# Optimization experiments

Hardware: AMD Instinct MI355X
Metric: run time of the kernel (lower is better)

## Reference

```python
import jax, jax.numpy as jnp
import numpy as np
import math

PATCH = 16
IMG = 224
HEADS = 12
EMB = 768
HEAD_DIM = EMB // HEADS
SCALE = 1.0 / math.sqrt(HEAD_DIM)
NEG = -1.0e9


def _make_masks():
    n = IMG // PATCH  # patches per side
    centers = np.arange(n) * PATCH + PATCH / 2.0
    rows = np.repeat(centers, n)  # token center rows, length n*n
    cols = np.tile(centers, n)    # token center cols
    left = (cols[:, None] < cols[None, :]).astype(np.float32)
    right = (cols[:, None] > cols[None, :]).astype(np.float32)
    up = (rows[:, None] < rows[None, :]).astype(np.float32)
    down = (rows[:, None] > rows[None, :]).astype(np.float32)
    ident = np.eye(n * n, dtype=np.float32)
    pad = lambda m: np.pad(m, ((1, 0), (1, 0)))  # prepend CLS row/col of zeros
    return [jnp.asarray(pad(m)) for m in (left, right, up, down, ident)]

MASKS = _make_masks()  # 5 masks, each [N, N] with N = 197


def setup_inputs() -> dict:
    key = jax.random.key(0)
    ks = jax.random.split(key, 18)
    B, N = 32, (IMG // PATCH) ** 2 + 1
    w = lambda k: jax.random.normal(k, (EMB, EMB), jnp.float32) * 0.02
    b = lambda k: jax.random.normal(k, (EMB,), jnp.float32) * 0.02
    return {
        'x': jax.random.normal(ks[0], (B, N, EMB), jnp.float32),
        'q_w': w(ks[1]), 'q_b': b(ks[2]),
        'kA_w': w(ks[3]), 'kA_b': b(ks[4]),
        'kB_w': w(ks[5]), 'kB_b': b(ks[6]),
        'kC_w': w(ks[7]), 'kC_b': b(ks[8]),
        'kD_w': w(ks[9]), 'kD_b': b(ks[10]),
        'kE_w': w(ks[11]), 'kE_b': b(ks[12]),
        'v_w': w(ks[13]), 'v_b': b(ks[14]),
        'proj_w': w(ks[15]), 'proj_b': b(ks[16]),
    }


def reference(x, q_w, q_b, kA_w, kA_b, kB_w, kB_b, kC_w, kC_b, kD_w, kD_b,
              kE_w, kE_b, v_w, v_b, proj_w, proj_b):
    B, N, _ = x.shape
    # torch Linear: y = x @ W.T + b; then [B,N,H,D] -> [B,H,N,D]
    lin = lambda w, b_: (x @ w.T + b_).reshape(B, N, HEADS, HEAD_DIM).transpose(0, 2, 1, 3)
    q = lin(q_w, q_b) * SCALE
    v = lin(v_w, v_b)
    out = jnp.zeros_like(v)
    k_params = [(kA_w, kA_b), (kB_w, kB_b), (kC_w, kC_b), (kD_w, kD_b), (kE_w, kE_b)]
    for (kw, kb), mask in zip(k_params, MASKS):
        k = lin(kw, kb)
        scores = jnp.einsum('bhnd,bhmd->bhnm', q, k) + (1.0 - mask) * NEG
        out = out + jnp.einsum('bhnm,bhmd->bhnd', jax.nn.softmax(scores, axis=-1), v)
    out = out.transpose(0, 2, 1, 3).reshape(B, N, EMB)
    return out @ proj_w.T + proj_b
```

## Files before the change

### kernel.cpp

```cpp
#include <hip/hip_runtime.h>
#include <stdint.h>

typedef unsigned short u16;
typedef __bf16 bf16x8 __attribute__((ext_vector_type(8)));
typedef float f32x4 __attribute__((ext_vector_type(4)));

#define KDIM   768
#define MP     6400
#define MREAL  6304
#define SLOT   ((size_t)MP * KDIM)
#define WSZ    ((size_t)KDIM * KDIM)
#define QSCALE_L 0.18033688011112042f
#define BIGL     1.4426950e9f

struct Ptr9 { const float* p[9]; };
struct Ptr7 { const float* p[7]; };

__device__ __forceinline__ u16 f2b(float f) {
  uint32_t x = __float_as_uint(f);
  x += 0x7FFFu + ((x >> 16) & 1u);
  return (u16)(x >> 16);
}

__device__ __forceinline__ float b2f(u16 v) {
  return __uint_as_float(((uint32_t)v) << 16);
}

__device__ __forceinline__ void async16(const void* g, void* l) {
  __builtin_amdgcn_global_load_lds(
      (__attribute__((address_space(1))) void*)(uintptr_t)g,
      (__attribute__((address_space(3))) void*)l, 16, 0, 0);
}

__global__ __launch_bounds__(256) void k_convert(Ptr9 src, u16* __restrict__ xb,
                                                 u16* __restrict__ wall) {
  const int XN4 = MREAL * KDIM / 4;
  const int WN4 = (int)(WSZ / 4);
  const int total = XN4 + 8 * WN4;
  for (int i = blockIdx.x * blockDim.x + threadIdx.x; i < total;
       i += gridDim.x * blockDim.x) {
    const float4* sp; ushort4* dp; int off;
    if (i < XN4) { sp = (const float4*)src.p[0]; dp = (ushort4*)xb; off = i; }
    else {
      int t = i - XN4; int slot = t / WN4; off = t - slot * WN4;
      sp = (const float4*)src.p[1 + slot];
      dp = (ushort4*)(wall + (size_t)slot * WSZ);
    }
    float4 v = sp[off];
    ushort4 u;
    u.x = f2b(v.x); u.y = f2b(v.y); u.z = f2b(v.z); u.w = f2b(v.w);
    dp[off] = u;
  }
}

__global__ __launch_bounds__(256) void k_gemm(const u16* __restrict__ A,
                                              const u16* __restrict__ W,
                                              Ptr7 bias,
                                              u16* __restrict__ outb,
                                              float* __restrict__ outf,
                                              float scale0, int guard) {
  __shared__ u16 As[128 * 32];
  __shared__ u16 Bs[128 * 32];
  const int tid = threadIdx.x;
  const int w = tid >> 6, lane = tid & 63;
  const int li = lane & 15, g = lane >> 4;
  const int brow = blockIdx.x, bcol = blockIdx.y, z = blockIdx.z;
  const u16* Wz = W + (size_t)z * WSZ;
  const float* bz = bias.p[z];
  const int wr = (w >> 1) * 64, wc = (w & 1) * 64;
  f32x4 acc[4][4] = {};

  for (int k0 = 0; k0 < KDIM; k0 += 32) {
    __syncthreads();
#pragma unroll
    for (int c = 0; c < 2; ++c) {
      int cbase = (c * 4 + w) * 64;
      int chunk = cbase + lane;
      int row = chunk >> 2, kg = chunk & 3;
      async16(A  + (size_t)(brow * 128 + row) * KDIM + k0 + kg * 8,
              (char*)As + cbase * 16);
      async16(Wz + (size_t)(bcol * 128 + row) * KDIM + k0 + kg * 8,
              (char*)Bs + cbase * 16);
    }
    asm volatile("s_waitcnt vmcnt(0)" ::: "memory");
    __syncthreads();

    bf16x8 af[4], bfr[4];
#pragma unroll
    for (int i = 0; i < 4; ++i) {
      af[i]  = *(const bf16x8*)(As + (wr + i * 16 + li) * 32 + g * 8);
      bfr[i] = *(const bf16x8*)(Bs + (wc + i * 16 + li) * 32 + g * 8);
    }
#pragma unroll
    for (int i = 0; i < 4; ++i)
#pragma unroll
      for (int j = 0; j < 4; ++j)
        acc[i][j] = __builtin_amdgcn_mfma_f32_16x16x32_bf16(af[i], bfr[j],
                                                            acc[i][j], 0, 0, 0);
  }

  const float scz = (z == 0) ? scale0 : 1.0f;
  if (outf == nullptr) {
    u16* O = outb + (size_t)z * SLOT;
#pragma unroll
    for (int j = 0; j < 4; ++j) {
      int col = bcol * 128 + wc + j * 16 + li;
      float bsv = bz[col];
#pragma unroll
      for (int i = 0; i < 4; ++i) {
        int row = brow * 128 + wr + i * 16 + g * 4;
#pragma unroll
        for (int r = 0; r < 4; ++r)
          O[(size_t)(row + r) * KDIM + col] = f2b((acc[i][j][r] + bsv) * scz);
      }
    }
  } else {
#pragma unroll
    for (int j = 0; j < 4; ++j) {
      int col = bcol * 128 + wc + j * 16 + li;
      float bsv = bz[col];
#pragma unroll
      for (int i = 0; i < 4; ++i) {
        int row = brow * 128 + wr + i * 16 + g * 4;
#pragma unroll
        for (int r = 0; r < 4; ++r)
          if (row + r < guard)
            outf[(size_t)(row + r) * KDIM + col] = acc[i][j][r] + bsv;
      }
    }
  }
}

__global__ __launch_bounds__(512, 4) void k_attn(const u16* __restrict__ qkv,
                                                 u16* __restrict__ att) {
  __shared__ u16 KL[208 * 64];
  __shared__ u16 VT[64][228];
  __shared__ u16 P[2][8][16][36];
  const int tid = threadIdx.x;
  const int w = tid >> 6, lane = tid & 63;
  const int li = lane & 15, g = lane >> 4;
  const int bx = blockIdx.x, h = blockIdx.y, b = blockIdx.z;
  const int rt = bx * 8 + w;
  const size_t rowbase = (size_t)b * 197;
  const int cb = h * 64;
  const u16* Q = qkv;
  const u16* V = qkv + 6 * SLOT;
  const bool task = (rt <= 12);
  const int nmask = (bx == 0) ? 5 : 4;

  auto stageK = [&](int m) {
    const u16* Kg = qkv + (size_t)(1 + m) * SLOT;
#pragma unroll
    for (int i = 0; i < 4; ++i) {
      int cb64 = (i * 8 + w) * 64;
      if (cb64 >= 1664) break;
      int c = cb64 + lane;
      int row = c >> 3;
      int kg = (c & 7) ^ (row & 7);
      async16(Kg + (rowbase + row) * KDIM + cb + kg * 8,
              (char*)KL + cb64 * 16);
    }
  };

  stageK(0);

  for (int e = tid; e < 64 * 228; e += 512) {
    int j = e >> 6, d = e & 63;
    u16 val = 0;
    if (j < 197) val = V[(rowbase + j) * KDIM + cb + d];
    VT[d][j] = val;
  }

  const int i_ = rt * 16 + li;
  const int pi = i_ - 1;
  const int ri = pi / 14, ci = pi % 14;
  const bool i0 = (i_ == 0);

  const int rs_init = (g * 4 - 1) / 14;
  const int cs_init = (g * 4 - 1) % 14;

  uint32_t b0l = 0, b0h = 0, b1l = 0, b1h = 0, b2l = 0, b2h = 0,
           b3l = 0, b3h = 0, b4l = 0, b4h = 0;
  {
    int cs = cs_init, rs = rs_init;
#pragma unroll
    for (int t = 0; t < 13; ++t) {
      int jv = t * 16 + g * 4;
      int cjr = cs, rjr = rs;
#pragma unroll
      for (int r = 0; r < 4; ++r) {
        const bool ok = (jv != 0) && !i0;
        const bool k0 = (ci < cjr) && ok;
        const bool k1 = (ci > cjr) && ok;
        const bool k2 = (ri < rjr) && ok;
        const bool k3 = (ri > rjr) && ok;
        const bool k4 = (i_ == jv) && ok;
        const int e = t * 4 + r;
        const uint32_t bit = 1u << (e & 31);
        if (e < 32) {
          b0l |= k0 ? bit : 0u; b1l |= k1 ? bit : 0u; b2l |= k2 ? bit : 0u;
          b3l |= k3 ? bit : 0u; b4l |= k4 ? bit : 0u;
        } else {
          b0h |= k0 ? bit : 0u; b1h |= k1 ? bit : 0u; b2h |= k2 ? bit : 0u;
          b3h |= k3 ? bit : 0u; b4h |= k4 ? bit : 0u;
        }
        ++jv; ++cjr; if (cjr == 14) { cjr = 0; ++rjr; }
      }
      cs += 2; ++rs; if (cs >= 14) { cs -= 14; ++rs; }
    }
  }

  bf16x8 qa0, qa1;
  {
    const size_t qrow = rowbase + (size_t)rt * 16 + li;
    qa0 = *(const bf16x8*)(Q + qrow * KDIM + cb + g * 8);
    qa1 = *(const bf16x8*)(Q + qrow * KDIM + cb + 32 + g * 8);
  }

  f32x4 oacc[4] = {};

  for (int m = 0; m < nmask; ++m) {
    asm volatile("s_waitcnt vmcnt(0)" ::: "memory");
    __syncthreads();

    const bool doit = task && (m < 4 || rt == 0);
    f32x4 s[13];
    if (doit) {
      __builtin_amdgcn_s_setprio(1);
#pragma unroll
      for (int t = 0; t < 13; ++t) {
        const char* base = (const char*)KL + (size_t)(t * 16 + li) * 128;
        const int sw = (li & 7) << 4;
        bf16x8 kb0 = *(const bf16x8*)(base + ((g * 16) ^ sw));
        bf16x8 kb1 = *(const bf16x8*)(base + ((64 + g * 16) ^ sw));
        f32x4 zz = {};
        zz = __builtin_amdgcn_mfma_f32_16x16x32_bf16(kb0, qa0, zz, 0, 0, 0);
        zz = __builtin_amdgcn_mfma_f32_16x16x32_bf16(kb1, qa1, zz, 0, 0, 0);
        s[t] = zz;
      }
      __builtin_amdgcn_s_setprio(0);
    }
    __syncthreads();
    if (m + 1 < nmask) stageK(m + 1);

    if (doit) {
      uint32_t wlo, whi;
      if (m == 0)      { wlo = b0l; whi = b0h; }
      else if (m == 1) { wlo = b1l; whi = b1h; }
      else if (m == 2) { wlo = b2l; whi = b2h; }
      else if (m == 3) { wlo = b3l; whi = b3h; }
      else             { wlo = b4l; whi = b4h; }

      float mx = -3.0e38f;
#pragma unroll
      for (int t = 0; t < 13; ++t) {
#pragma unroll
        for (int r = 0; r < 4; ++r) {
          const int e = t * 4 + r;
          const uint32_t w32 = (e < 32) ? wlo : whi;
          const bool mk = ((w32 >> (e & 31)) & 1u) != 0u;
          const int jv = t * 16 + g * 4 + r;
          float sv = s[t][r] - (mk ? 0.f : BIGL);
          if (jv >= 197) sv = -3.0e38f;
          s[t][r] = sv;
          mx = fmaxf(mx, sv);
        }
      }
      mx = fmaxf(mx, __shfl_xor(mx, 16));
      mx = fmaxf(mx, __shfl_xor(mx, 32));
      float sum = 0.f;
#pragma unroll
      for (int t = 0; t < 13; ++t)
#pragma unroll
        for (int r = 0; r < 4; ++r) {
          float e_ = exp2f(s[t][r] - mx);
          s[t][r] = e_;
          sum += e_;
        }
      sum += __shfl_xor(sum, 16);
      sum += __shfl_xor(sum, 32);
      const float inv = 1.0f / sum;

#pragma unroll
      for (int kt = 0; kt <= 7; ++kt) {
        if (kt < 7) {
#pragma unroll
          for (int h2 = 0; h2 < 2; ++h2) {
            const int t = kt * 2 + h2;
            uint32_t w0 = 0, w1 = 0;
            if (t < 13) {
              float a0 = s[t][0] * inv, a1 = s[t][1] * inv;
              float a2 = s[t][2] * inv, a3 = s[t][3] * inv;
              asm("v_cvt_pk_bf16_f32 %0, %1, %2" : "=v"(w0) : "v"(a0), "v"(a1));
              asm("v_cvt_pk_bf16_f32 %0, %1, %2" : "=v"(w1) : "v"(a2), "v"(a3));
            }
            uint2 pw; pw.x = w0; pw.y = w1;
            *(uint2*)&P[kt & 1][w][li][h2 * 16 + g * 4] = pw;
          }
        }
        if (kt > 0) {
          const int kr = kt - 1;
          bf16x8 pa = *(const bf16x8*)&P[kr & 1][w][li][g * 8];
          __builtin_amdgcn_s_setprio(1);
#pragma unroll
          for (int dt = 0; dt < 4; ++dt) {
            bf16x8 vb = *(const bf16x8*)&VT[dt * 16 + li][kr * 32 + g * 8];
            oacc[dt] = __builtin_amdgcn_mfma_f32_16x16x32_bf16(pa, vb, oacc[dt],
                                                               0, 0, 0);
          }
          __builtin_amdgcn_s_setprio(0);
        }
      }
    }
  }

  if (task && rt > 0) {
#pragma unroll
    for (int dt = 0; dt < 4; ++dt)
#pragma unroll
      for (int r = 0; r < 4; ++r) {
        int i2 = rt * 16 + g * 4 + r;
        oacc[dt][r] += b2f(VT[dt * 16 + li][i2]);
      }
  }

  if (task) {
#pragma unroll
    for (int dt = 0; dt < 4; ++dt)
#pragma unroll
      for (int r = 0; r < 4; ++r) {
        int i2 = rt * 16 + g * 4 + r;
        if (i2 < 197)
          att[(rowbase + i2) * KDIM + cb + dt * 16 + li] = f2b(oacc[dt][r]);
      }
  }
}

extern "C" void kernel_launch(void* const* d_in, const int* in_sizes, int n_in,
                              void* d_out, int out_size, void* d_ws, size_t ws_size,
                              hipStream_t stream) {
  (void)in_sizes; (void)n_in; (void)out_size; (void)ws_size;
  const float* x      = (const float*)d_in[0];
  const float* q_w    = (const float*)d_in[1];
  const float* q_b    = (const float*)d_in[2];
  const float* kA_w   = (const float*)d_in[3];
  const float* kA_b   = (const float*)d_in[4];
  const float* kB_w   = (const float*)d_in[5];
  const float* kB_b   = (const float*)d_in[6];
  const float* kC_w   = (const float*)d_in[7];
  const float* kC_b   = (const float*)d_in[8];
  const float* kD_w   = (const float*)d_in[9];
  const float* kD_b   = (const float*)d_in[10];
  const float* kE_w   = (const float*)d_in[11];
  const float* kE_b   = (const float*)d_in[12];
  const float* v_w    = (const float*)d_in[13];
  const float* v_b    = (const float*)d_in[14];
  const float* proj_w = (const float*)d_in[15];
  const float* proj_b = (const float*)d_in[16];
  float* out = (float*)d_out;

  u16* xb   = (u16*)d_ws;
  u16* qkv  = xb + SLOT;
  u16* wall = qkv + 7 * SLOT;
  u16* att  = xb;

  Ptr9 cs;
  cs.p[0] = x;    cs.p[1] = q_w;  cs.p[2] = kA_w; cs.p[3] = kB_w;
  cs.p[4] = kC_w; cs.p[5] = kD_w; cs.p[6] = kE_w; cs.p[7] = v_w;
  cs.p[8] = proj_w;
  k_convert<<<dim3(2048), dim3(256), 0, stream>>>(cs, xb, wall);

  Ptr7 b1;
  b1.p[0] = q_b;  b1.p[1] = kA_b; b1.p[2] = kB_b; b1.p[3] = kC_b;
  b1.p[4] = kD_b; b1.p[5] = kE_b; b1.p[6] = v_b;
  k_gemm<<<dim3(50, 6, 7), dim3(256), 0, stream>>>(xb, wall, b1, qkv, nullptr,
                                                   QSCALE_L, 0);

  k_attn<<<dim3(2, 12, 32), dim3(512), 0, stream>>>(qkv, att);

  Ptr7 b2;
  for (int i = 0; i < 7; ++i) b2.p[i] = proj_b;
  k_gemm<<<dim3(50, 6, 1), dim3(256), 0, stream>>>(att, wall + 7 * WSZ, b2,
                                                   nullptr, out, 1.0f, MREAL);
}
```

Before: 199.6 us.

## Feed softmax probabilities to MFMA from registers via permuted V layout

Removes the shared-memory P staging buffer that reshaped softmax probabilities into MFMA A-operand layout. Instead the V transpose in LDS is stored with a permuted key order, so the per-lane score registers can be packed straight into the bf16x8 A operand. This drops the LDS write/read round trip per k-step and the P buffer's shared memory. Launch bounds are relaxed from 4 to 2 blocks per CU, which gives the compiler more registers per thread but may allow fewer resident waves.

```diff
diff --git a/kernel.cpp b/kernel.cpp
--- a/kernel.cpp
+++ b/kernel.cpp
@@ -131,11 +131,10 @@
   }
 }
 
-__global__ __launch_bounds__(512, 4) void k_attn(const u16* __restrict__ qkv,
+__global__ __launch_bounds__(512, 2) void k_attn(const u16* __restrict__ qkv,
                                                  u16* __restrict__ att) {
   __shared__ u16 KL[208 * 64];
   __shared__ u16 VT[64][228];
-  __shared__ u16 P[2][8][16][36];
   const int tid = threadIdx.x;
   const int w = tid >> 6, lane = tid & 63;
   const int li = lane & 15, g = lane >> 4;
@@ -164,11 +163,13 @@
 
   stageK(0);
 
-  for (int e = tid; e < 64 * 228; e += 512) {
+  for (int e = tid; e < 64 * 224; e += 512) {
     int j = e >> 6, d = e & 63;
     u16 val = 0;
     if (j < 197) val = V[(rowbase + j) * KDIM + cb + d];
-    VT[d][j] = val;
+    int t = j >> 4;
+    int kp = (t >> 1) * 32 + ((j >> 2) & 3) * 8 + (t & 1) * 4 + (j & 3);
+    VT[d][kp] = val;
   }
 
   const int i_ = rt * 16 + li;
@@ -281,35 +282,30 @@
       sum += __shfl_xor(sum, 32);
       const float inv = 1.0f / sum;
 
-#pragma unroll
-      for (int kt = 0; kt <= 7; ++kt) {
-        if (kt < 7) {
-#pragma unroll
-          for (int h2 = 0; h2 < 2; ++h2) {
-            const int t = kt * 2 + h2;
-            uint32_t w0 = 0, w1 = 0;
-            if (t < 13) {
-              float a0 = s[t][0] * inv, a1 = s[t][1] * inv;
-              float a2 = s[t][2] * inv, a3 = s[t][3] * inv;
-              asm("v_cvt_pk_bf16_f32 %0, %1, %2" : "=v"(w0) : "v"(a0), "v"(a1));
-              asm("v_cvt_pk_bf16_f32 %0, %1, %2" : "=v"(w1) : "v"(a2), "v"(a3));
-            }
-            uint2 pw; pw.x = w0; pw.y = w1;
-            *(uint2*)&P[kt & 1][w][li][h2 * 16 + g * 4] = pw;
-          }
-        }
-        if (kt > 0) {
-          const int kr = kt - 1;
-          bf16x8 pa = *(const bf16x8*)&P[kr & 1][w][li][g * 8];
-          __builtin_amdgcn_s_setprio(1);
-#pragma unroll
-          for (int dt = 0; dt < 4; ++dt) {
-            bf16x8 vb = *(const bf16x8*)&VT[dt * 16 + li][kr * 32 + g * 8];
-            oacc[dt] = __builtin_amdgcn_mfma_f32_16x16x32_bf16(pa, vb, oacc[dt],
-                                                               0, 0, 0);
-          }
-          __builtin_amdgcn_s_setprio(0);
-        }
+      union PU { uint32_t u[4]; bf16x8 v; };
+#pragma unroll
+      for (int kt = 0; kt < 7; ++kt) {
+        PU pu;
+        {
+          float a0 = s[2 * kt][0] * inv, a1 = s[2 * kt][1] * inv;
+          float a2 = s[2 * kt][2] * inv, a3 = s[2 * kt][3] * inv;
+          asm("v_cvt_pk_bf16_f32 %0, %1, %2" : "=v"(pu.u[0]) : "v"(a0), "v"(a1));
+          asm("v_cvt_pk_bf16_f32 %0, %1, %2" : "=v"(pu.u[1]) : "v"(a2), "v"(a3));
+        }
+        if (kt < 6) {
+          float c0 = s[2 * kt + 1][0] * inv, c1 = s[2 * kt + 1][1] * inv;
+          float c2 = s[2 * kt + 1][2] * inv, c3 = s[2 * kt + 1][3] * inv;
+          asm("v_cvt_pk_bf16_f32 %0, %1, %2" : "=v"(pu.u[2]) : "v"(c0), "v"(c1));
+          asm("v_cvt_pk_bf16_f32 %0, %1, %2" : "=v"(pu.u[3]) : "v"(c2), "v"(c3));
+        } else { pu.u[2] = 0; pu.u[3] = 0; }
+        __builtin_amdgcn_s_setprio(1);
+#pragma unroll
+        for (int dt = 0; dt < 4; ++dt) {
+          bf16x8 vb = *(const bf16x8*)&VT[dt * 16 + li][kt * 32 + g * 8];
+          oacc[dt] = __builtin_amdgcn_mfma_f32_16x16x32_bf16(pu.v, vb,
+                                                             oacc[dt], 0, 0, 0);
+        }
+        __builtin_amdgcn_s_setprio(0);
       }
     }
   }
@@ -320,7 +316,9 @@
 #pragma unroll
       for (int r = 0; r < 4; ++r) {
         int i2 = rt * 16 + g * 4 + r;
-        oacc[dt][r] += b2f(VT[dt * 16 + li][i2]);
+        int t2 = i2 >> 4;
+        int k2 = (t2 >> 1) * 32 + ((i2 >> 2) & 3) * 8 + (t2 & 1) * 4 + (i2 & 3);
+        oacc[dt][r] += b2f(VT[dt * 16 + li][k2]);
       }
   }
 
```

After: 219.9 us. +10.2%, slower.
